# Kernel tuning notes

Measured on AMD Instinct MI355X. Metric: run time of the kernel, lower is better.

## Reference

```python
import jax, jax.numpy as jnp
import numpy as np

WT, WX = 101, 11
SIGMA_TAU, SIGMA_HX = 21.0, 11.0
EPS = 1e-9


def _gauss1d(n, sigma):
    xx = jnp.arange(n, dtype=jnp.float32) - n // 2
    k = jnp.exp(-(xx ** 2) / (2.0 * sigma ** 2))
    return k / k.sum()


def _smooth(img, k_t, k_x):
    # img: [B, 1, T, X]; separable Gaussian window (exact: 2D kernel is outer product)
    dn = ('NCHW', 'OIHW', 'NCHW')
    out = jax.lax.conv_general_dilated(img, k_t.reshape(1, 1, -1, 1), (1, 1), 'SAME', dimension_numbers=dn)
    out = jax.lax.conv_general_dilated(out, k_x.reshape(1, 1, 1, -1), (1, 1), 'SAME', dimension_numbers=dn)
    return out


def setup_inputs() -> dict:
    key = jax.random.key(0)
    kx, ky = jax.random.split(key)
    shape = (16, 1, 2500, 512)
    return {
        'x': jax.random.normal(kx, shape, dtype=jnp.float32),
        'y': jax.random.normal(ky, shape, dtype=jnp.float32),
    }


def reference(x, y):
    k_t = _gauss1d(WT, SIGMA_TAU)
    k_x = _gauss1d(WX, SIGMA_HX)
    mu_x = _smooth(x, k_t, k_x)
    mu_y = _smooth(y, k_t, k_x)
    var_x = _smooth(x * x, k_t, k_x) - mu_x * mu_x
    var_y = _smooth(y * y, k_t, k_x) - mu_y * mu_y
    cov_xy = _smooth(x * y, k_t, k_x) - mu_x * mu_y
    # normalized local coherence map in [-1, 1]
    cs = cov_xy * jax.lax.rsqrt(var_x * var_y + EPS)
    return (1.0 - cs).mean()
```

## Files before the change

### kernel.cpp

```cpp
#include <hip/hip_runtime.h>

#define B_   16
#define T_   2500
#define X_   512
#define XT   32
#define SEGS 4
#define SEGR 640
#define NSX  (X_ / XT)
#define NBLK (B_ * SEGS * NSX)
#define RING 20

typedef __attribute__((ext_vector_type(4))) float f32x4;

__device__ __forceinline__ void barrier_lgkm() {
    asm volatile("s_waitcnt lgkmcnt(0)\n\ts_barrier" ::: "memory");
}

__global__ __launch_bounds__(256, 4) void coh11(const float* __restrict__ xg,
                                                const float* __restrict__ yg,
                                                float* __restrict__ partial)
{
    __shared__ float ktn[104];
    __shared__ float kxn[12];
    __shared__ float norm2[2];
    __shared__ unsigned long long XS[RING][5][34];
    __shared__ unsigned long long PBq[2][5][16][9];
    __shared__ float wred[4];

    const int tid  = threadIdx.x;
    const int lane = tid & 63;
    const int w    = tid >> 6;
    const int g    = lane >> 4;
    const int ln16 = lane & 15;
    const int p01  = w & 1;

    const int bid = blockIdx.x;
    const int wid = (bid & 7) * (NBLK / 8) + (bid >> 3);
    const int xt  = wid & 15;
    const int seg = (wid >> 4) & 3;
    const int b   = wid >> 6;

    const int pair = ((w >> 1) ^ wid) & 1;

    const int x0    = xt * XT;
    const int t0    = seg * SEGR;
    const int t_end = min(t0 + SEGR, T_);
    const int nm    = (t_end - t0 + 15) >> 4;
    const int pmax  = nm + 9;

    if (tid < 104) ktn[tid] = 0.0f;
    if (tid < 12)  kxn[tid] = 0.0f;
    __syncthreads();
    if (tid < 101) { float d = (float)(tid - 50); ktn[tid] = expf(-d * d / (2.0f * 21.0f * 21.0f)); }
    if (tid < 11)  { float d = (float)(tid - 5);  kxn[tid] = expf(-d * d / (2.0f * 11.0f * 11.0f)); }
    __syncthreads();
    if (tid == 0) {
        float s = 0.f; for (int i = 0; i < 101; ++i) s += ktn[i]; norm2[0] = 1.0f / s;
        s = 0.f;       for (int i = 0; i < 11;  ++i) s += kxn[i]; norm2[1] = 1.0f / s;
    }
    __syncthreads();
    if (tid < 101) ktn[tid] *= norm2[0];
    if (tid < 11)  kxn[tid] *= norm2[1];
    __syncthreads();

    const float* xb = xg + (size_t)b * T_ * X_;
    const float* yb = yg + (size_t)b * T_ * X_;

    float local = 0.f;

    if (pair == 0) {
        long a_x;
        {
            float vv[8];
#pragma unroll
            for (int sl = 0; sl < 8; ++sl) {
                int idx = 8 * g + sl - ln16 - 3;
                vv[sl] = (idx >= 0 && idx <= 10) ? kxn[idx] * 16.0f : 0.0f;
            }
            int lo = __builtin_amdgcn_cvt_pk_fp8_f32(vv[0], vv[1], 0, false);
            lo     = __builtin_amdgcn_cvt_pk_fp8_f32(vv[2], vv[3], lo, true);
            int hi = __builtin_amdgcn_cvt_pk_fp8_f32(vv[4], vv[5], 0, false);
            hi     = __builtin_amdgcn_cvt_pk_fp8_f32(vv[6], vv[7], hi, true);
            a_x = (long)(((unsigned long long)(unsigned)hi << 32) | (unsigned)lo);
        }
        const uint sel1  = (ln16 & 1) ? 0x07030602u : 0x01050004u;
        const uint sel2  = (ln16 & 2) ? 0x07060302u : 0x01000504u;
        const int  cidx  = ((ln16 & 1) << 1) | ((ln16 >> 1) & 1);
        const int  abyte = (ln16 & 4);
        const int  uhalf = (ln16 >> 3);

        const int  gcol  = x0 - 16 + 4 * ln16;
        const bool colOK = (gcol >= 0) && (gcol < X_);

        float4 xv[2], yv[2];
#pragma unroll
        for (int s = 0; s < 2; ++s) {
            int grow = t0 - 56 + 8 * p01 + 4 * s + g;
            bool ok = colOK && (grow >= 0) && (grow < T_);
            xv[s] = ok ? *(const float4*)(xb + (size_t)grow * X_ + gcol) : make_float4(0.f, 0.f, 0.f, 0.f);
            yv[s] = ok ? *(const float4*)(yb + (size_t)grow * X_ + gcol) : make_float4(0.f, 0.f, 0.f, 0.f);
        }

        int gb = 0;
        for (int it = 0; it <= pmax; ++it) {
            if (it >= 1 && it <= nm + 7) {
                int u0 = gb + 18; if (u0 >= RING) u0 -= RING;
                const int uu = u0 + uhalf;
                const int sb = (it - 1) & 1;
#pragma unroll
                for (int f = 0; f < 5; ++f) {
                    long bfrag = (long)PBq[sb][f][ln16][1 + 2 * p01 + g];
                    f32x4 z; z[0] = 0.f; z[1] = 0.f; z[2] = 0.f; z[3] = 0.f;
                    f32x4 d = __builtin_amdgcn_mfma_f32_16x16x32_fp8_fp8(a_x, bfrag, z, 0, 0, 0);
                    int pk = __builtin_amdgcn_cvt_pk_fp8_f32(d[0], d[1], 0, false);
                    pk     = __builtin_amdgcn_cvt_pk_fp8_f32(d[2], d[3], pk, true);
                    uint pkc   = (uint)pk;
                    uint part1 = (uint)__builtin_amdgcn_update_dpp(0, (int)pkc, 177, 0xF, 0xF, true);
                    uint s1v   = __builtin_amdgcn_perm(pkc, part1, sel1);
                    uint part2 = (uint)__builtin_amdgcn_update_dpp(0, (int)s1v, 78, 0xF, 0xF, true);
                    uint Tt    = __builtin_amdgcn_perm(s1v, part2, sel2);
                    *(uint*)((uchar*)&XS[uu][f][16 * p01 + 4 * g + cidx] + abyte) = Tt;
                }
            }
            if (it <= nm + 6) {
                const int db = it & 1;
#pragma unroll
                for (int s = 0; s < 2; ++s) {
                    int rrs = 8 * p01 + 4 * s + g;
                    float4 X = xv[s], Y = yv[s];
                    int q0 = __builtin_amdgcn_cvt_pk_fp8_f32(X.x, X.y, 0, false);
                    q0     = __builtin_amdgcn_cvt_pk_fp8_f32(X.z, X.w, q0, true);
                    int q1 = __builtin_amdgcn_cvt_pk_fp8_f32(Y.x, Y.y, 0, false);
                    q1     = __builtin_amdgcn_cvt_pk_fp8_f32(Y.z, Y.w, q1, true);
                    int q2 = __builtin_amdgcn_cvt_pk_fp8_f32(X.x * X.x, X.y * X.y, 0, false);
                    q2     = __builtin_amdgcn_cvt_pk_fp8_f32(X.z * X.z, X.w * X.w, q2, true);
                    int q3 = __builtin_amdgcn_cvt_pk_fp8_f32(Y.x * Y.x, Y.y * Y.y, 0, false);
                    q3     = __builtin_amdgcn_cvt_pk_fp8_f32(Y.z * Y.z, Y.w * Y.w, q3, true);
                    int q4 = __builtin_amdgcn_cvt_pk_fp8_f32(X.x * Y.x, X.y * Y.y, 0, false);
                    q4     = __builtin_amdgcn_cvt_pk_fp8_f32(X.z * Y.z, X.w * Y.w, q4, true);
                    *(uint*)((uchar*)&PBq[db][0][rrs][0] + 4 * ln16) = (uint)q0;
                    *(uint*)((uchar*)&PBq[db][1][rrs][0] + 4 * ln16) = (uint)q1;
                    *(uint*)((uchar*)&PBq[db][2][rrs][0] + 4 * ln16) = (uint)q2;
                    *(uint*)((uchar*)&PBq[db][3][rrs][0] + 4 * ln16) = (uint)q3;
                    *(uint*)((uchar*)&PBq[db][4][rrs][0] + 4 * ln16) = (uint)q4;
                }
            }
            if (it + 1 <= nm + 6) {
#pragma unroll
                for (int s = 0; s < 2; ++s) {
                    int grow = t0 - 56 + 16 * (it + 1) + 8 * p01 + 4 * s + g;
                    bool ok = colOK && (grow >= 0) && (grow < T_);
                    xv[s] = ok ? *(const float4*)(xb + (size_t)grow * X_ + gcol) : make_float4(0.f, 0.f, 0.f, 0.f);
                    yv[s] = ok ? *(const float4*)(yb + (size_t)grow * X_ + gcol) : make_float4(0.f, 0.f, 0.f, 0.f);
                }
            }
            barrier_lgkm();
            gb += 2; if (gb >= RING) gb -= RING;
        }
    } else {
        long a_t[4];
#pragma unroll
        for (int c = 0; c < 4; ++c) {
            float vv[8];
#pragma unroll
            for (int sl = 0; sl < 8; ++sl) {
                int idx = 32 * c + 8 * g + sl - ln16 - 6;
                vv[sl] = (idx >= 0 && idx <= 100) ? ktn[idx] * 16.0f : 0.0f;
            }
            int lo = __builtin_amdgcn_cvt_pk_fp8_f32(vv[0], vv[1], 0, false);
            lo     = __builtin_amdgcn_cvt_pk_fp8_f32(vv[2], vv[3], lo, true);
            int hi = __builtin_amdgcn_cvt_pk_fp8_f32(vv[4], vv[5], 0, false);
            hi     = __builtin_amdgcn_cvt_pk_fp8_f32(vv[6], vv[7], hi, true);
            a_t[c] = (long)(((unsigned long long)(unsigned)hi << 32) | (unsigned)lo);
        }

        int gb = 0;
        for (int it = 0; it <= pmax; ++it) {
            if (it >= 10) {
                const int m = it - 10;
                long bf0[5], bf1[5], bf2[5], bf3[5];
                {
                    int u0 = gb + g;      if (u0 >= RING) u0 -= RING;
                    int u1 = gb + 4 + g;  if (u1 >= RING) u1 -= RING;
                    int u2 = gb + 8 + g;  if (u2 >= RING) u2 -= RING;
                    int u3 = gb + 12 + g; if (u3 >= RING) u3 -= RING;
                    const int nn = 16 * p01 + ln16;
#pragma unroll
                    for (int f = 0; f < 5; ++f) bf0[f] = (long)XS[u0][f][nn];
#pragma unroll
                    for (int f = 0; f < 5; ++f) bf1[f] = (long)XS[u1][f][nn];
#pragma unroll
                    for (int f = 0; f < 5; ++f) bf2[f] = (long)XS[u2][f][nn];
#pragma unroll
                    for (int f = 0; f < 5; ++f) bf3[f] = (long)XS[u3][f][nn];
                }
                f32x4 acc[5];
#pragma unroll
                for (int f = 0; f < 5; ++f) { acc[f][0] = 0.f; acc[f][1] = 0.f; acc[f][2] = 0.f; acc[f][3] = 0.f; }
#pragma unroll
                for (int f = 0; f < 5; ++f) acc[f] = __builtin_amdgcn_mfma_f32_16x16x32_fp8_fp8(a_t[0], bf0[f], acc[f], 0, 0, 0);
#pragma unroll
                for (int f = 0; f < 5; ++f) acc[f] = __builtin_amdgcn_mfma_f32_16x16x32_fp8_fp8(a_t[1], bf1[f], acc[f], 0, 0, 0);
#pragma unroll
                for (int f = 0; f < 5; ++f) acc[f] = __builtin_amdgcn_mfma_f32_16x16x32_fp8_fp8(a_t[2], bf2[f], acc[f], 0, 0, 0);
#pragma unroll
                for (int f = 0; f < 5; ++f) acc[f] = __builtin_amdgcn_mfma_f32_16x16x32_fp8_fp8(a_t[3], bf3[f], acc[f], 0, 0, 0);

                const float s_ = 1.0f / 256.0f;
#pragma unroll
                for (int r = 0; r < 4; ++r) {
                    int t = t0 + 16 * m + 4 * g + r;
                    if (t < t_end) {
                        float a0 = acc[0][r], a1 = acc[1][r];
                        float sa0 = a0 * s_, sa1 = a1 * s_;
                        float cov = fmaf(-sa0, a1, acc[4][r]);
                        float vx  = fmaf(-sa0, a0, acc[2][r]);
                        float vy  = fmaf(-sa1, a1, acc[3][r]);
                        local += 1.0f - cov * rsqrtf(fmaf(vx, vy, 6.5536e-5f));
                    }
                }
            }
            barrier_lgkm();
            gb += 2; if (gb >= RING) gb -= RING;
        }
    }

#pragma unroll
    for (int off = 32; off >= 1; off >>= 1) local += __shfl_down(local, off);
    if ((tid & 63) == 0) wred[tid >> 6] = local;
    __syncthreads();
    if (tid == 0)
        partial[wid] = wred[0] + wred[1] + wred[2] + wred[3];
}

__global__ __launch_bounds__(256) void coh_reduce(const float* __restrict__ partial,
                                                  float* __restrict__ out) {
    __shared__ float wred[4];
    const int tid = threadIdx.x;
    float s = 0.0f;
    for (int i = tid; i < NBLK; i += 256) s += partial[i];
#pragma unroll
    for (int off = 32; off >= 1; off >>= 1) s += __shfl_down(s, off);
    if ((tid & 63) == 0) wred[tid >> 6] = s;
    __syncthreads();
    if (tid == 0)
        out[0] = (wred[0] + wred[1] + wred[2] + wred[3]) *
                 (1.0f / ((float)B_ * (float)T_ * (float)X_));
}

extern "C" void kernel_launch(void* const* d_in, const int* in_sizes, int n_in,
                              void* d_out, int out_size, void* d_ws, size_t ws_size,
                              hipStream_t stream) {
    const float* x = (const float*)d_in[0];
    const float* y = (const float*)d_in[1];
    float* out = (float*)d_out;
    float* partial = (float*)d_ws;

    coh11<<<dim3(NBLK), 256, 0, stream>>>(x, y, partial);
    coh_reduce<<<1, 256, 0, stream>>>(partial, out);
}
```

Measured before the change: 62.01 us.

## Split time into five segments, single-buffer P stage, and fast-path interior loads

Changes the time split from 4 segments of 640 rows to 5 of 512, giving 1280 blocks and raising launch bounds to 5 blocks per CU for better occupancy and load balance. The PB staging buffer drops double buffering and the XS ring shrinks, cutting the pipeline depth by one iteration and reducing LDS so more blocks fit. Interior tiles skip the per-row boundary checks on global loads and in the final reduction. The risks are more halo rows re-read per segment, and the single-buffered PB relying on the barrier ordering to avoid read/write hazards.

```diff
diff --git a/kernel.cpp b/kernel.cpp
--- a/kernel.cpp
+++ b/kernel.cpp
@@ -4,11 +4,11 @@
 #define T_   2500
 #define X_   512
 #define XT   32
-#define SEGS 4
-#define SEGR 640
+#define SEGS 5
+#define SEGR 512
 #define NSX  (X_ / XT)
 #define NBLK (B_ * SEGS * NSX)
-#define RING 20
+#define RING 18
 
 typedef __attribute__((ext_vector_type(4))) float f32x4;
 
@@ -16,15 +16,15 @@
     asm volatile("s_waitcnt lgkmcnt(0)\n\ts_barrier" ::: "memory");
 }
 
-__global__ __launch_bounds__(256, 4) void coh11(const float* __restrict__ xg,
+__global__ __launch_bounds__(256, 5) void coh12(const float* __restrict__ xg,
                                                 const float* __restrict__ yg,
                                                 float* __restrict__ partial)
 {
     __shared__ float ktn[104];
     __shared__ float kxn[12];
     __shared__ float norm2[2];
-    __shared__ unsigned long long XS[RING][5][34];
-    __shared__ unsigned long long PBq[2][5][16][9];
+    __shared__ unsigned long long XS[RING][5][32];
+    __shared__ unsigned long long PB[5][16][8];
     __shared__ float wred[4];
 
     const int tid  = threadIdx.x;
@@ -37,8 +37,9 @@
     const int bid = blockIdx.x;
     const int wid = (bid & 7) * (NBLK / 8) + (bid >> 3);
     const int xt  = wid & 15;
-    const int seg = (wid >> 4) & 3;
-    const int b   = wid >> 6;
+    const int hi5 = wid >> 4;
+    const int seg = hi5 % SEGS;
+    const int b   = hi5 / SEGS;
 
     const int pair = ((w >> 1) ^ wid) & 1;
 
@@ -46,7 +47,7 @@
     const int t0    = seg * SEGR;
     const int t_end = min(t0 + SEGR, T_);
     const int nm    = (t_end - t0 + 15) >> 4;
-    const int pmax  = nm + 9;
+    const int pmax  = nm + 8;
 
     if (tid < 104) ktn[tid] = 0.0f;
     if (tid < 12)  kxn[tid] = 0.0f;
@@ -87,29 +88,45 @@
         const uint sel2  = (ln16 & 2) ? 0x07060302u : 0x01000504u;
         const int  cidx  = ((ln16 & 1) << 1) | ((ln16 >> 1) & 1);
         const int  abyte = (ln16 & 4);
-        const int  uhalf = (ln16 >> 3);
+        const int  hh    = ln16 >> 3;
+        const int  prow  = 8 * p01 + (ln16 & 7);
 
         const int  gcol  = x0 - 16 + 4 * ln16;
         const bool colOK = (gcol >= 0) && (gcol < X_);
+        const float* xpl = xb + gcol;
+        const float* ypl = yb + gcol;
+        const float4 z4  = make_float4(0.f, 0.f, 0.f, 0.f);
 
         float4 xv[2], yv[2];
-#pragma unroll
-        for (int s = 0; s < 2; ++s) {
-            int grow = t0 - 56 + 8 * p01 + 4 * s + g;
-            bool ok = colOK && (grow >= 0) && (grow < T_);
-            xv[s] = ok ? *(const float4*)(xb + (size_t)grow * X_ + gcol) : make_float4(0.f, 0.f, 0.f, 0.f);
-            yv[s] = ok ? *(const float4*)(yb + (size_t)grow * X_ + gcol) : make_float4(0.f, 0.f, 0.f, 0.f);
-        }
+        auto issue_loads = [&](int c) {
+            const int rowlo = t0 - 56 + 16 * c;
+            if (rowlo >= 0 && rowlo + 15 < T_) {
+#pragma unroll
+                for (int s = 0; s < 2; ++s) {
+                    int grow = rowlo + 8 * p01 + 4 * s + g;
+                    xv[s] = colOK ? *(const float4*)(xpl + (size_t)grow * X_) : z4;
+                    yv[s] = colOK ? *(const float4*)(ypl + (size_t)grow * X_) : z4;
+                }
+            } else {
+#pragma unroll
+                for (int s = 0; s < 2; ++s) {
+                    int grow = rowlo + 8 * p01 + 4 * s + g;
+                    bool ok = colOK && (grow >= 0) && (grow < T_);
+                    xv[s] = ok ? *(const float4*)(xpl + (size_t)grow * X_) : z4;
+                    yv[s] = ok ? *(const float4*)(ypl + (size_t)grow * X_) : z4;
+                }
+            }
+        };
+        issue_loads(0);
 
         int gb = 0;
         for (int it = 0; it <= pmax; ++it) {
             if (it >= 1 && it <= nm + 7) {
-                int u0 = gb + 18; if (u0 >= RING) u0 -= RING;
-                const int uu = u0 + uhalf;
-                const int sb = (it - 1) & 1;
+                int u0 = gb + 16; if (u0 >= RING) u0 -= RING;
+                const int uu = u0 + p01;
 #pragma unroll
                 for (int f = 0; f < 5; ++f) {
-                    long bfrag = (long)PBq[sb][f][ln16][1 + 2 * p01 + g];
+                    long bfrag = (long)PB[f][prow][1 + 2 * hh + g];
                     f32x4 z; z[0] = 0.f; z[1] = 0.f; z[2] = 0.f; z[3] = 0.f;
                     f32x4 d = __builtin_amdgcn_mfma_f32_16x16x32_fp8_fp8(a_x, bfrag, z, 0, 0, 0);
                     int pk = __builtin_amdgcn_cvt_pk_fp8_f32(d[0], d[1], 0, false);
@@ -119,11 +136,10 @@
                     uint s1v   = __builtin_amdgcn_perm(pkc, part1, sel1);
                     uint part2 = (uint)__builtin_amdgcn_update_dpp(0, (int)s1v, 78, 0xF, 0xF, true);
                     uint Tt    = __builtin_amdgcn_perm(s1v, part2, sel2);
-                    *(uint*)((uchar*)&XS[uu][f][16 * p01 + 4 * g + cidx] + abyte) = Tt;
+                    *(uint*)((uchar*)&XS[uu][f][16 * hh + 4 * g + cidx] + abyte) = Tt;
                 }
             }
             if (it <= nm + 6) {
-                const int db = it & 1;
 #pragma unroll
                 for (int s = 0; s < 2; ++s) {
                     int rrs = 8 * p01 + 4 * s + g;
@@ -138,22 +154,14 @@
                     q3     = __builtin_amdgcn_cvt_pk_fp8_f32(Y.z * Y.z, Y.w * Y.w, q3, true);
                     int q4 = __builtin_amdgcn_cvt_pk_fp8_f32(X.x * Y.x, X.y * Y.y, 0, false);
                     q4     = __builtin_amdgcn_cvt_pk_fp8_f32(X.z * Y.z, X.w * Y.w, q4, true);
-                    *(uint*)((uchar*)&PBq[db][0][rrs][0] + 4 * ln16) = (uint)q0;
-                    *(uint*)((uchar*)&PBq[db][1][rrs][0] + 4 * ln16) = (uint)q1;
-                    *(uint*)((uchar*)&PBq[db][2][rrs][0] + 4 * ln16) = (uint)q2;
-                    *(uint*)((uchar*)&PBq[db][3][rrs][0] + 4 * ln16) = (uint)q3;
-                    *(uint*)((uchar*)&PBq[db][4][rrs][0] + 4 * ln16) = (uint)q4;
-                }
-            }
-            if (it + 1 <= nm + 6) {
-#pragma unroll
-                for (int s = 0; s < 2; ++s) {
-                    int grow = t0 - 56 + 16 * (it + 1) + 8 * p01 + 4 * s + g;
-                    bool ok = colOK && (grow >= 0) && (grow < T_);
-                    xv[s] = ok ? *(const float4*)(xb + (size_t)grow * X_ + gcol) : make_float4(0.f, 0.f, 0.f, 0.f);
-                    yv[s] = ok ? *(const float4*)(yb + (size_t)grow * X_ + gcol) : make_float4(0.f, 0.f, 0.f, 0.f);
-                }
-            }
+                    *(uint*)((uchar*)&PB[0][rrs][0] + 4 * ln16) = (uint)q0;
+                    *(uint*)((uchar*)&PB[1][rrs][0] + 4 * ln16) = (uint)q1;
+                    *(uint*)((uchar*)&PB[2][rrs][0] + 4 * ln16) = (uint)q2;
+                    *(uint*)((uchar*)&PB[3][rrs][0] + 4 * ln16) = (uint)q3;
+                    *(uint*)((uchar*)&PB[4][rrs][0] + 4 * ln16) = (uint)q4;
+                }
+            }
+            if (it + 1 <= nm + 6) issue_loads(it + 1);
             barrier_lgkm();
             gb += 2; if (gb >= RING) gb -= RING;
         }
@@ -176,8 +184,8 @@
 
         int gb = 0;
         for (int it = 0; it <= pmax; ++it) {
-            if (it >= 10) {
-                const int m = it - 10;
+            if (it >= 9) {
+                const int m = it - 9;
                 long bf0[5], bf1[5], bf2[5], bf3[5];
                 {
                     int u0 = gb + g;      if (u0 >= RING) u0 -= RING;
@@ -207,10 +215,9 @@
                 for (int f = 0; f < 5; ++f) acc[f] = __builtin_amdgcn_mfma_f32_16x16x32_fp8_fp8(a_t[3], bf3[f], acc[f], 0, 0, 0);
 
                 const float s_ = 1.0f / 256.0f;
-#pragma unroll
-                for (int r = 0; r < 4; ++r) {
-                    int t = t0 + 16 * m + 4 * g + r;
-                    if (t < t_end) {
+                if (16 * m + 15 < t_end - t0) {
+#pragma unroll
+                    for (int r = 0; r < 4; ++r) {
                         float a0 = acc[0][r], a1 = acc[1][r];
                         float sa0 = a0 * s_, sa1 = a1 * s_;
                         float cov = fmaf(-sa0, a1, acc[4][r]);
@@ -218,6 +225,19 @@
                         float vy  = fmaf(-sa1, a1, acc[3][r]);
                         local += 1.0f - cov * rsqrtf(fmaf(vx, vy, 6.5536e-5f));
                     }
+                } else {
+#pragma unroll
+                    for (int r = 0; r < 4; ++r) {
+                        int t = t0 + 16 * m + 4 * g + r;
+                        if (t < t_end) {
+                            float a0 = acc[0][r], a1 = acc[1][r];
+                            float sa0 = a0 * s_, sa1 = a1 * s_;
+                            float cov = fmaf(-sa0, a1, acc[4][r]);
+                            float vx  = fmaf(-sa0, a0, acc[2][r]);
+                            float vy  = fmaf(-sa1, a1, acc[3][r]);
+                            local += 1.0f - cov * rsqrtf(fmaf(vx, vy, 6.5536e-5f));
+                        }
+                    }
                 }
             }
             barrier_lgkm();
@@ -256,6 +276,6 @@
     float* out = (float*)d_out;
     float* partial = (float*)d_ws;
 
-    coh11<<<dim3(NBLK), 256, 0, stream>>>(x, y, partial);
+    coh12<<<dim3(NBLK), 256, 0, stream>>>(x, y, partial);
     coh_reduce<<<1, 256, 0, stream>>>(partial, out);
 }
```

New measurement: 89.81 us. 1.45x slower.
